# Optimization experiments

Hardware: AMD Instinct MI355X
Metric: run time of the kernel (lower is better)

The kernel has to match this reference:

```python
import jax, jax.numpy as jnp
import numpy as np

N, E, F_IN, F_OUT = 50000, 640000, 128, 128


def setup_inputs() -> dict:
    key = jax.random.key(0)
    k_x, k_w, k_b = jax.random.split(key, 3)
    x = jax.random.normal(k_x, (N, F_IN), dtype=jnp.float32)
    # Unique directed edges so segment_sum == dense spmm with adj[u,v]=1.
    rng = np.random.default_rng(0)
    lin = np.unique(rng.integers(0, N * N, size=2 * E, dtype=np.int64))[:E]
    edge_index = jnp.stack([jnp.asarray(lin // N), jnp.asarray(lin % N)]).astype(jnp.int64)
    stdv = 1.0 / np.sqrt(F_OUT).astype(np.float32)
    weight = jax.random.uniform(k_w, (F_IN, F_OUT), dtype=jnp.float32, minval=-stdv, maxval=stdv)
    bias = jax.random.uniform(k_b, (F_OUT,), dtype=jnp.float32, minval=-stdv, maxval=stdv)
    return {"input": x, "edge_index": edge_index, "weight": weight, "bias": bias}


def reference(input, edge_index, weight, bias):
    # support = X @ W  [N, F_OUT]
    support = input @ weight
    # Dense adj with adj[u,v]=1 followed by spmm(adj, support) is, for unique
    # edges, exactly: out[u] = sum_{(u,v) in edges} support[v]
    u, v = edge_index[0], edge_index[1]
    out = jax.ops.segment_sum(support[v], u, num_segments=input.shape[0])
    return out + bias
```

## Files before the change

### kernel.cpp

```cpp
#include <hip/hip_runtime.h>
#include <stdint.h>


typedef __attribute__((ext_vector_type(8))) short bf16x8;
typedef __attribute__((ext_vector_type(4))) float f32x4;

#define WSTRIDE 136

__device__ __forceinline__ unsigned short f2bf(float f) {
    union { float f; uint32_t u; } c; c.f = f;
    uint32_t u = c.u;
    uint32_t r = (u + 0x7FFFu + ((u >> 16) & 1u)) >> 16;
    return (unsigned short)r;
}
__device__ __forceinline__ float bf2f(unsigned short u) {
    union { uint32_t u; float f; } c; c.u = ((uint32_t)u) << 16;
    return c.f;
}

__global__ __launch_bounds__(256)
void gcn_setup(const int* __restrict__ eu, const float* __restrict__ W,
               int* __restrict__ row_ptr, unsigned short* __restrict__ Wg,
               int N, int E)
{
    const int g = blockIdx.x * 256 + threadIdx.x;
    if (g < E) {
        int cur  = eu[g];
        int prev = (g > 0) ? eu[g - 1] : -1;
        for (int r = prev + 1; r <= cur; ++r) row_ptr[r] = g;
    }
    if (g <= N) {
        int last = eu[E - 1];
        if (g > last) row_ptr[g] = E;
    }
    if (g < 16384) {
        int k = g >> 7, n = g & 127;
        Wg[n * 128 + k] = f2bf(W[g]);
    }
}

__global__ __launch_bounds__(256)
void gcn_cast(const float* __restrict__ x, unsigned short* __restrict__ xb, int n8)
{
    const int g = blockIdx.x * 256 + threadIdx.x;
    if (g < n8) {
        const float4* x4 = (const float4*)x;
        float4 a = x4[2 * g], b = x4[2 * g + 1];
        union { unsigned short u[8]; uint4 v; } pk;
        pk.u[0] = f2bf(a.x); pk.u[1] = f2bf(a.y); pk.u[2] = f2bf(a.z); pk.u[3] = f2bf(a.w);
        pk.u[4] = f2bf(b.x); pk.u[5] = f2bf(b.y); pk.u[6] = f2bf(b.z); pk.u[7] = f2bf(b.w);
        ((uint4*)xb)[g] = pk.v;
    }
}

template<bool BF>
__global__ __launch_bounds__(256)
void gcn_main(const float* __restrict__ x,
              const unsigned short* __restrict__ xb,
              const int* __restrict__ ev,
              const int* __restrict__ row_ptr,
              const unsigned short* __restrict__ Wg,
              const float* __restrict__ bias,
              float* __restrict__ out,
              int N, int E, int TW)
{
    __shared__ __align__(16) unsigned short At[16 * WSTRIDE];

    const int t    = threadIdx.x;
    const int wid  = t >> 6;
    const int lane = t & 63;
    const int quad = lane >> 4;
    const int l15  = lane & 15;

    const int wg = blockIdx.x * 4 + wid;

    int bnd;
    {
        const int m = (lane >> 1) & 3, e = lane & 1;
        bnd = row_ptr[min(wg + m * TW + e, N)];
    }

    unsigned short* Am = At + (wid * 4) * WSTRIDE;

    int vIdx = ev[min(__shfl(bnd, 0) + lane, E - 1)];

    for (int m = 0; m < 4; ++m) {
        const int s = __shfl(bnd, 2 * m);
        const int c = __shfl(bnd, 2 * m + 1) - s;
        int vNext = (m < 3) ? ev[min(__shfl(bnd, 2 * m + 2) + lane, E - 1)] : 0;

        if constexpr (BF) {
            const int eslot = lane >> 4;
            const int fo = l15 * 8;
            float fa[8];
            #pragma unroll
            for (int i = 0; i < 8; ++i) fa[i] = 0.f;

            for (int base = 0; base < c; base += 32) {
                if (base && ((base & 63) == 0))
                    vIdx = ev[min(s + base + lane, E - 1)];
                bf16x8 tv[8];
                float  sc[8];
                #pragma unroll
                for (int k = 0; k < 8; ++k) {
                    const int eidx = base + k * 4 + eslot;
                    int v = __shfl(vIdx, eidx & 63);
                    const bool act = (eidx < c);
                    sc[k] = act ? 1.0f : 0.0f;
                    v = act ? v : 0;
                    tv[k] = *(const bf16x8*)(xb + (size_t)v * 128 + fo);
                }
                #pragma unroll
                for (int k = 0; k < 8; ++k)
                    #pragma unroll
                    for (int i = 0; i < 8; ++i)
                        fa[i] = fmaf(bf2f((unsigned short)tv[k][i]), sc[k], fa[i]);
            }
            #pragma unroll
            for (int i = 0; i < 8; ++i) {
                fa[i] += __shfl_xor(fa[i], 16);
                fa[i] += __shfl_xor(fa[i], 32);
            }
            if (eslot == 0) {
                union { unsigned short u[8]; uint4 v; } pk;
                #pragma unroll
                for (int i = 0; i < 8; ++i) pk.u[i] = f2bf(fa[i]);
                *(uint4*)(Am + m * WSTRIDE + fo) = pk.v;
            }
        } else {
            const int half = lane >> 5;
            const int l31  = lane & 31;
            const float4* x4 = (const float4*)x;
            const float4 fz = {0.f, 0.f, 0.f, 0.f};
            float4 a0 = fz, a1 = fz;
            for (int base = 0; base < c; base += 16) {
                if (base && ((base & 63) == 0))
                    vIdx = ev[min(s + base + lane, E - 1)];
                float4 tv[8];
                float  sc[8];
                #pragma unroll
                for (int k = 0; k < 8; ++k) {
                    const int eidx = base + 2 * k + half;
                    int v = __shfl(vIdx, eidx & 63);
                    const bool act = (eidx < c);
                    sc[k] = act ? 1.0f : 0.0f;
                    v = act ? v : 0;
                    tv[k] = x4[((long long)v << 5) + l31];
                }
                #pragma unroll
                for (int k = 0; k < 8; ++k) {
                    float4& a = (k & 1) ? a1 : a0;
                    a.x = fmaf(tv[k].x, sc[k], a.x);
                    a.y = fmaf(tv[k].y, sc[k], a.y);
                    a.z = fmaf(tv[k].z, sc[k], a.z);
                    a.w = fmaf(tv[k].w, sc[k], a.w);
                }
            }
            a0.x += a1.x; a0.y += a1.y; a0.z += a1.z; a0.w += a1.w;
            a0.x += __shfl_xor(a0.x, 32);
            a0.y += __shfl_xor(a0.y, 32);
            a0.z += __shfl_xor(a0.z, 32);
            a0.w += __shfl_xor(a0.w, 32);
            if (half == 0) {
                ushort4 pk;
                pk.x = f2bf(a0.x); pk.y = f2bf(a0.y);
                pk.z = f2bf(a0.z); pk.w = f2bf(a0.w);
                *(ushort4*)(Am + m * WSTRIDE + 4 * l31) = pk;
            }
        }
        vIdx = vNext;
    }
    __syncthreads();

    f32x4 acc[2];
    #pragma unroll
    for (int nt = 0; nt < 2; ++nt) { acc[nt].x = 0.f; acc[nt].y = 0.f; acc[nt].z = 0.f; acc[nt].w = 0.f; }

    #pragma unroll
    for (int ks = 0; ks < 4; ++ks) {
        const int kofs = ks * 32 + quad * 8;
        bf16x8 a = *(const bf16x8*)(At + l15 * WSTRIDE + kofs);
        #pragma unroll
        for (int nt = 0; nt < 2; ++nt) {
            const int col = wid * 32 + nt * 16 + l15;
            bf16x8 b = *(const bf16x8*)(Wg + col * 128 + kofs);
            acc[nt] = __builtin_amdgcn_mfma_f32_16x16x32_bf16(a, b, acc[nt], 0, 0, 0);
        }
    }

    const int b4 = blockIdx.x * 4;
    #pragma unroll
    for (int nt = 0; nt < 2; ++nt) {
        const int col = wid * 32 + nt * 16 + l15;
        const float bcol = bias[col];
        #pragma unroll
        for (int r = 0; r < 4; ++r) {
            const int mi  = quad * 4 + r;
            const int row = b4 + (mi >> 2) + (mi & 3) * TW;
            if (row < N)
                __builtin_nontemporal_store(acc[nt][r] + bcol,
                                            &out[(long long)row * 128 + col]);
        }
    }
}

extern "C" void kernel_launch(void* const* d_in, const int* in_sizes, int n_in,
                              void* d_out, int out_size, void* d_ws, size_t ws_size,
                              hipStream_t stream) {
    const float* x    = (const float*)d_in[0];
    const int*   ei   = (const int*)d_in[1];
    const float* W    = (const float*)d_in[2];
    const float* bias = (const float*)d_in[3];
    float*       out  = (float*)d_out;

    const int N = in_sizes[0] / 128;
    const int E = in_sizes[1] / 2;

    const size_t rp_b   = ((size_t)(N + 1) * 4 + 255) & ~(size_t)255;
    const size_t wg_off = rp_b;
    const size_t xb_off = (wg_off + 32768 + 255) & ~(size_t)255;
    const size_t xb_b   = (size_t)N * 128 * 2;

    int*            row_ptr = (int*)d_ws;
    unsigned short* Wg      = (unsigned short*)((char*)d_ws + wg_off);
    unsigned short* xb      = (unsigned short*)((char*)d_ws + xb_off);
    const bool use_bf = (ws_size >= xb_off + xb_b);

    const int setup_threads = (E > N + 1 ? E : N + 1);
    gcn_setup<<<(setup_threads + 255) / 256, 256, 0, stream>>>(ei, W, row_ptr, Wg, N, E);

    const int grid = (N + 15) / 16;
    const int TW   = grid * 4;
    if (use_bf) {
        const int n8 = N * 16;
        gcn_cast<<<(n8 + 255) / 256, 256, 0, stream>>>(x, xb, n8);
        gcn_main<true><<<grid, 256, 0, stream>>>(x, xb, ei + E, row_ptr, Wg, bias, out, N, E, TW);
    } else {
        gcn_main<false><<<grid, 256, 0, stream>>>(x, xb, ei + E, row_ptr, Wg, bias, out, N, E, TW);
    }
}
```

Measured before the change: 124.8 us.

## Merge prep kernels, use contiguous row blocks, double-buffer gathers, skip empty blocks

Folds the setup and bf16 cast kernels into one prep launch, which removes a kernel launch. The main kernel now gives each block 16 contiguous rows instead of a strided interleave. It prefetches the first 32 neighbour rows of the next destination row while the current one is accumulated, using two register buffers. Blocks whose rows have no edges write only the bias and exit early. The fp32 fallback path for a small workspace is removed, so the code now assumes the workspace always fits the bf16 copy, and the doubled gather buffers raise register pressure.

Measured after the change: 112.1 us. 1.11x faster.

```diff
diff --git a/kernel.cpp b/kernel.cpp
--- a/kernel.cpp
+++ b/kernel.cpp
@@ -19,28 +19,10 @@
 }
 
 __global__ __launch_bounds__(256)
-void gcn_setup(const int* __restrict__ eu, const float* __restrict__ W,
-               int* __restrict__ row_ptr, unsigned short* __restrict__ Wg,
-               int N, int E)
-{
-    const int g = blockIdx.x * 256 + threadIdx.x;
-    if (g < E) {
-        int cur  = eu[g];
-        int prev = (g > 0) ? eu[g - 1] : -1;
-        for (int r = prev + 1; r <= cur; ++r) row_ptr[r] = g;
-    }
-    if (g <= N) {
-        int last = eu[E - 1];
-        if (g > last) row_ptr[g] = E;
-    }
-    if (g < 16384) {
-        int k = g >> 7, n = g & 127;
-        Wg[n * 128 + k] = f2bf(W[g]);
-    }
-}
-
-__global__ __launch_bounds__(256)
-void gcn_cast(const float* __restrict__ x, unsigned short* __restrict__ xb, int n8)
+void gcn_prep(const float* __restrict__ x, const int* __restrict__ eu,
+              const float* __restrict__ W,
+              int* __restrict__ row_ptr, unsigned short* __restrict__ Wg,
+              unsigned short* __restrict__ xb, int N, int E, int n8)
 {
     const int g = blockIdx.x * 256 + threadIdx.x;
     if (g < n8) {
@@ -51,124 +33,129 @@
         pk.u[4] = f2bf(b.x); pk.u[5] = f2bf(b.y); pk.u[6] = f2bf(b.z); pk.u[7] = f2bf(b.w);
         ((uint4*)xb)[g] = pk.v;
     }
-}
-
-template<bool BF>
+    if (g < E) {
+        int cur  = eu[g];
+        int prev = (g > 0) ? eu[g - 1] : -1;
+        for (int r = prev + 1; r <= cur; ++r) row_ptr[r] = g;
+    }
+    if (g <= N) {
+        int last = eu[E - 1];
+        if (g > last) row_ptr[g] = E;
+    }
+    if (g < 16384) {
+        int k = g >> 7, n = g & 127;
+        Wg[n * 128 + k] = f2bf(W[g]);
+    }
+}
+
 __global__ __launch_bounds__(256)
-void gcn_main(const float* __restrict__ x,
-              const unsigned short* __restrict__ xb,
+void gcn_main(const unsigned short* __restrict__ xb,
               const int* __restrict__ ev,
               const int* __restrict__ row_ptr,
               const unsigned short* __restrict__ Wg,
               const float* __restrict__ bias,
               float* __restrict__ out,
-              int N, int E, int TW)
+              int N, int E)
 {
     __shared__ __align__(16) unsigned short At[16 * WSTRIDE];
 
-    const int t    = threadIdx.x;
-    const int wid  = t >> 6;
-    const int lane = t & 63;
-    const int quad = lane >> 4;
-    const int l15  = lane & 15;
-
-    const int wg = blockIdx.x * 4 + wid;
-
-    int bnd;
-    {
-        const int m = (lane >> 1) & 3, e = lane & 1;
-        bnd = row_ptr[min(wg + m * TW + e, N)];
-    }
-
-    unsigned short* Am = At + (wid * 4) * WSTRIDE;
-
-    int vIdx = ev[min(__shfl(bnd, 0) + lane, E - 1)];
-
+    const int t     = threadIdx.x;
+    const int wid   = t >> 6;
+    const int lane  = t & 63;
+    const int quad  = lane >> 4;
+    const int l15   = lane & 15;
+    const int eslot = lane >> 4;
+    const int fo    = l15 * 8;
+
+    const int r0 = blockIdx.x * 16;
+
+    int bnd = row_ptr[min(r0 + (lane < 17 ? lane : 16), N)];
+
+    if (__shfl(bnd, 0) == __shfl(bnd, 16)) {
+        const f32x4* b4 = (const f32x4*)bias;
+        f32x4*       o4 = (f32x4*)out;
+        #pragma unroll
+        for (int i = 0; i < 2; ++i) {
+            const int f   = i * 256 + t;
+            const int row = r0 + (f >> 5);
+            if (row < N)
+                __builtin_nontemporal_store(b4[f & 31], &o4[(size_t)row * 32 + (f & 31)]);
+        }
+        return;
+    }
+
+    int sA[4], cA[4], vI[4];
+    #pragma unroll
     for (int m = 0; m < 4; ++m) {
-        const int s = __shfl(bnd, 2 * m);
-        const int c = __shfl(bnd, 2 * m + 1) - s;
-        int vNext = (m < 3) ? ev[min(__shfl(bnd, 2 * m + 2) + lane, E - 1)] : 0;
-
-        if constexpr (BF) {
-            const int eslot = lane >> 4;
-            const int fo = l15 * 8;
-            float fa[8];
+        sA[m] = __shfl(bnd, wid * 4 + m);
+        cA[m] = __shfl(bnd, wid * 4 + m + 1) - sA[m];
+    }
+    #pragma unroll
+    for (int m = 0; m < 4; ++m)
+        vI[m] = ev[min(sA[m] + lane, E - 1)];
+
+    bf16x8 tv[2][8];
+
+    if (cA[0] > 0) {
+        #pragma unroll
+        for (int k = 0; k < 8; ++k) {
+            const int v = __shfl(vI[0], k * 4 + eslot);
+            tv[0][k] = *(const bf16x8*)(xb + (size_t)v * 128 + fo);
+        }
+    }
+
+    #pragma unroll
+    for (int m = 0; m < 4; ++m) {
+        const int buf = m & 1;
+        if (m < 3 && cA[m + 1] > 0) {
             #pragma unroll
-            for (int i = 0; i < 8; ++i) fa[i] = 0.f;
-
-            for (int base = 0; base < c; base += 32) {
-                if (base && ((base & 63) == 0))
-                    vIdx = ev[min(s + base + lane, E - 1)];
-                bf16x8 tv[8];
-                float  sc[8];
+            for (int k = 0; k < 8; ++k) {
+                const int v = __shfl(vI[m + 1], k * 4 + eslot);
+                tv[(m + 1) & 1][k] = *(const bf16x8*)(xb + (size_t)v * 128 + fo);
+            }
+        }
+
+        float fa[8];
+        #pragma unroll
+        for (int i = 0; i < 8; ++i) fa[i] = 0.f;
+
+        if (cA[m] > 0) {
+            #pragma unroll
+            for (int k = 0; k < 8; ++k) {
+                const float s = (k * 4 + eslot < cA[m]) ? 1.0f : 0.0f;
+                #pragma unroll
+                for (int i = 0; i < 8; ++i)
+                    fa[i] = fmaf(bf2f((unsigned short)tv[buf][k][i]), s, fa[i]);
+            }
+            for (int base = 32; base < cA[m]; base += 32) {
+                if ((base & 63) == 0)
+                    vI[m] = ev[min(sA[m] + base + lane, E - 1)];
                 #pragma unroll
                 for (int k = 0; k < 8; ++k) {
-                    const int eidx = base + k * 4 + eslot;
-                    int v = __shfl(vIdx, eidx & 63);
-                    const bool act = (eidx < c);
-                    sc[k] = act ? 1.0f : 0.0f;
-                    v = act ? v : 0;
-                    tv[k] = *(const bf16x8*)(xb + (size_t)v * 128 + fo);
-                }
-                #pragma unroll
-                for (int k = 0; k < 8; ++k)
-                    #pragma unroll
-                    for (int i = 0; i < 8; ++i)
-                        fa[i] = fmaf(bf2f((unsigned short)tv[k][i]), sc[k], fa[i]);
-            }
-            #pragma unroll
-            for (int i = 0; i < 8; ++i) {
-                fa[i] += __shfl_xor(fa[i], 16);
-                fa[i] += __shfl_xor(fa[i], 32);
-            }
-            if (eslot == 0) {
-                union { unsigned short u[8]; uint4 v; } pk;
-                #pragma unroll
-                for (int i = 0; i < 8; ++i) pk.u[i] = f2bf(fa[i]);
-                *(uint4*)(Am + m * WSTRIDE + fo) = pk.v;
-            }
-        } else {
-            const int half = lane >> 5;
-            const int l31  = lane & 31;
-            const float4* x4 = (const float4*)x;
-            const float4 fz = {0.f, 0.f, 0.f, 0.f};
-            float4 a0 = fz, a1 = fz;
-            for (int base = 0; base < c; base += 16) {
-                if (base && ((base & 63) == 0))
-                    vIdx = ev[min(s + base + lane, E - 1)];
-                float4 tv[8];
-                float  sc[8];
-                #pragma unroll
-                for (int k = 0; k < 8; ++k) {
-                    const int eidx = base + 2 * k + half;
-                    int v = __shfl(vIdx, eidx & 63);
-                    const bool act = (eidx < c);
-                    sc[k] = act ? 1.0f : 0.0f;
-                    v = act ? v : 0;
-                    tv[k] = x4[((long long)v << 5) + l31];
+                    const int v = __shfl(vI[m], (base + k * 4 + eslot) & 63);
+                    tv[buf][k] = *(const bf16x8*)(xb + (size_t)v * 128 + fo);
                 }
                 #pragma unroll
                 for (int k = 0; k < 8; ++k) {
-                    float4& a = (k & 1) ? a1 : a0;
-                    a.x = fmaf(tv[k].x, sc[k], a.x);
-                    a.y = fmaf(tv[k].y, sc[k], a.y);
-                    a.z = fmaf(tv[k].z, sc[k], a.z);
-                    a.w = fmaf(tv[k].w, sc[k], a.w);
+                    const float s = (base + k * 4 + eslot < cA[m]) ? 1.0f : 0.0f;
+                    #pragma unroll
+                    for (int i = 0; i < 8; ++i)
+                        fa[i] = fmaf(bf2f((unsigned short)tv[buf][k][i]), s, fa[i]);
                 }
             }
-            a0.x += a1.x; a0.y += a1.y; a0.z += a1.z; a0.w += a1.w;
-            a0.x += __shfl_xor(a0.x, 32);
-            a0.y += __shfl_xor(a0.y, 32);
-            a0.z += __shfl_xor(a0.z, 32);
-            a0.w += __shfl_xor(a0.w, 32);
-            if (half == 0) {
-                ushort4 pk;
-                pk.x = f2bf(a0.x); pk.y = f2bf(a0.y);
-                pk.z = f2bf(a0.z); pk.w = f2bf(a0.w);
-                *(ushort4*)(Am + m * WSTRIDE + 4 * l31) = pk;
-            }
-        }
-        vIdx = vNext;
+        }
+
+        #pragma unroll
+        for (int i = 0; i < 8; ++i) {
+            fa[i] += __shfl_xor(fa[i], 16);
+            fa[i] += __shfl_xor(fa[i], 32);
+        }
+        if (eslot == 0) {
+            union { unsigned short u[8]; uint4 v; } pk;
+            #pragma unroll
+            for (int i = 0; i < 8; ++i) pk.u[i] = f2bf(fa[i]);
+            *(uint4*)(At + (wid * 4 + m) * WSTRIDE + fo) = pk.v;
+        }
     }
     __syncthreads();
 
@@ -188,15 +175,13 @@
         }
     }
 
-    const int b4 = blockIdx.x * 4;
     #pragma unroll
     for (int nt = 0; nt < 2; ++nt) {
         const int col = wid * 32 + nt * 16 + l15;
         const float bcol = bias[col];
         #pragma unroll
         for (int r = 0; r < 4; ++r) {
-            const int mi  = quad * 4 + r;
-            const int row = b4 + (mi >> 2) + (mi & 3) * TW;
+            const int row = r0 + quad * 4 + r;
             if (row < N)
                 __builtin_nontemporal_store(acc[nt][r] + bcol,
                                             &out[(long long)row * 128 + col]);
@@ -219,23 +204,16 @@
     const size_t rp_b   = ((size_t)(N + 1) * 4 + 255) & ~(size_t)255;
     const size_t wg_off = rp_b;
     const size_t xb_off = (wg_off + 32768 + 255) & ~(size_t)255;
-    const size_t xb_b   = (size_t)N * 128 * 2;
 
     int*            row_ptr = (int*)d_ws;
     unsigned short* Wg      = (unsigned short*)((char*)d_ws + wg_off);
     unsigned short* xb      = (unsigned short*)((char*)d_ws + xb_off);
-    const bool use_bf = (ws_size >= xb_off + xb_b);
-
-    const int setup_threads = (E > N + 1 ? E : N + 1);
-    gcn_setup<<<(setup_threads + 255) / 256, 256, 0, stream>>>(ei, W, row_ptr, Wg, N, E);
+
+    const int n8 = N * 16;
+    int prep_threads = n8 > E ? n8 : E;
+    if (prep_threads < N + 1) prep_threads = N + 1;
+    gcn_prep<<<(prep_threads + 255) / 256, 256, 0, stream>>>(x, ei, W, row_ptr, Wg, xb, N, E, n8);
 
     const int grid = (N + 15) / 16;
-    const int TW   = grid * 4;
-    if (use_bf) {
-        const int n8 = N * 16;
-        gcn_cast<<<(n8 + 255) / 256, 256, 0, stream>>>(x, xb, n8);
-        gcn_main<true><<<grid, 256, 0, stream>>>(x, xb, ei + E, row_ptr, Wg, bias, out, N, E, TW);
-    } else {
-        gcn_main<false><<<grid, 256, 0, stream>>>(x, xb, ei + E, row_ptr, Wg, bias, out, N, E, TW);
-    }
-}
+    gcn_main<<<grid, 256, 0, stream>>>(xb, ei + E, row_ptr, Wg, bias, out, N, E);
+}
```
